# Kernel tuning notes

Measured on AMD Instinct MI355X. Metric: run time of the kernel, lower is better.

Reference implementation:

```python
import jax, jax.numpy as jnp
import numpy as np

N_NODES = 100000
N_EDGES = 1000000
F_IN = 8
HID = 64
VOCAB = 64
TXT_F = 64
SEQ = 10
N_CLASSES = 2


def setup_inputs() -> dict:
    key = jax.random.key(0)
    ks = jax.random.split(key, 16)
    inp = {
        "x": jax.random.normal(ks[0], (N_NODES, F_IN), dtype=jnp.float32),
        "edge_index": jax.random.randint(ks[1], (2, N_EDGES), 0, N_NODES, dtype=jnp.int32),
        "xtext": jax.random.randint(ks[2], (N_NODES, SEQ), 0, VOCAB, dtype=jnp.int32),
        # GCN layers (PyG convention: out = norm_agg(x @ W) + b)
        "conv1_w": jax.random.normal(ks[3], (F_IN, HID), dtype=jnp.float32) * 0.2,
        "conv1_b": jnp.zeros((HID,), jnp.float32),
        "conv2_w": jax.random.normal(ks[4], (HID, HID), dtype=jnp.float32) * 0.1,
        "conv2_b": jnp.zeros((HID,), jnp.float32),
        # embedding + GRU (torch layout: w_ih [3H, in], w_hh [3H, H])
        "embed": jax.random.normal(ks[5], (VOCAB, TXT_F), dtype=jnp.float32) * 0.1,
        "gru_w_ih": jax.random.normal(ks[6], (3 * HID, TXT_F), dtype=jnp.float32) * 0.1,
        "gru_w_hh": jax.random.normal(ks[7], (3 * HID, HID), dtype=jnp.float32) * 0.1,
        "gru_b_ih": jnp.zeros((3 * HID,), jnp.float32),
        "gru_b_hh": jnp.zeros((3 * HID,), jnp.float32),
        # pair MLPs (torch Linear layout: [out, in])
        "lin1_w": jax.random.normal(ks[8], (HID, 2 * HID), dtype=jnp.float32) * 0.1,
        "lin1_b": jnp.zeros((HID,), jnp.float32),
        "lin_text_w": jax.random.normal(ks[9], (HID, 2 * HID), dtype=jnp.float32) * 0.1,
        "lin_text_b": jnp.zeros((HID,), jnp.float32),
        "lin_final_w": jax.random.normal(ks[10], (N_CLASSES, 2 * HID), dtype=jnp.float32) * 0.1,
        "lin_final_b": jnp.zeros((N_CLASSES,), jnp.float32),
    }
    return inp


def _gcn_norm(edge_index, n_nodes):
    # PyG GCNConv default: add self loops, symmetric normalization
    loops = jnp.arange(n_nodes, dtype=edge_index.dtype)
    src = jnp.concatenate([edge_index[0], loops])
    dst = jnp.concatenate([edge_index[1], loops])
    deg = jax.ops.segment_sum(jnp.ones_like(dst, dtype=jnp.float32), dst, num_segments=n_nodes)
    dinv = jnp.where(deg > 0, jax.lax.rsqrt(deg), 0.0)
    norm = dinv[src] * dinv[dst]  # [E+N]
    return src, dst, norm


def _gcn(h, src, dst, norm, W, b, n_nodes):
    h = h @ W                              # [N, out]
    msg = h[src] * norm[:, None]           # gather + scale
    out = jax.ops.segment_sum(msg, dst, num_segments=n_nodes)
    return out + b


def _gru_last(xe, w_ih, w_hh, b_ih, b_hh):
    # xe: [N, T, F]; returns last hidden state [N, H]
    H = w_hh.shape[1]
    gi_all = jnp.einsum('ntf,gf->ntg', xe, w_ih) + b_ih  # precompute input gates [N,T,3H]
    gi_all = jnp.transpose(gi_all, (1, 0, 2))            # [T, N, 3H]

    def step(h, gi):
        gh = h @ w_hh.T + b_hh
        i_r, i_z, i_n = jnp.split(gi, 3, axis=-1)
        h_r, h_z, h_n = jnp.split(gh, 3, axis=-1)
        r = jax.nn.sigmoid(i_r + h_r)
        z = jax.nn.sigmoid(i_z + h_z)
        n = jnp.tanh(i_n + r * h_n)
        h = (1.0 - z) * n + z * h
        return h, None

    h0 = jnp.zeros((xe.shape[0], H), xe.dtype)
    h_last, _ = jax.lax.scan(step, h0, gi_all)
    return h_last


def reference(x, edge_index, xtext,
              conv1_w, conv1_b, conv2_w, conv2_b,
              embed, gru_w_ih, gru_w_hh, gru_b_ih, gru_b_hh,
              lin1_w, lin1_b, lin_text_w, lin_text_b, lin_final_w, lin_final_b):
    n = x.shape[0]
    src, dst, norm = _gcn_norm(edge_index, n)

    h = jax.nn.relu(_gcn(x, src, dst, norm, conv1_w, conv1_b, n))
    h = jax.nn.relu(_gcn(h, src, dst, norm, conv2_w, conv2_b, n))

    xe = embed[xtext]                                   # [N, T, F]
    textout = _gru_last(xe, gru_w_ih, gru_w_hh, gru_b_ih, gru_b_hh)  # [N, 64]

    s, t = edge_index[0], edge_index[1]
    xpair = jnp.concatenate([h[s], h[t]], axis=1)       # [E, 128]
    xpair = jax.nn.relu(xpair @ lin1_w.T + lin1_b)

    xpairtext = jnp.concatenate([textout[s], textout[t]], axis=1)
    xpairtext = jax.nn.relu(xpairtext @ lin_text_w.T + lin_text_b)

    xfin = jnp.concatenate([xpair, xpairtext], axis=1) @ lin_final_w.T + lin_final_b
    return jax.nn.log_softmax(xfin, axis=1)
```

## Files before the change

kernel.cpp:

```cpp
#include <hip/hip_runtime.h>
#include <stdint.h>

#define N_NODES 100000
#define N_EDGES 1000000
#define NBLK 391

typedef unsigned short u16;
typedef unsigned int u32;
typedef __attribute__((ext_vector_type(8))) short bshort8;
typedef __attribute__((ext_vector_type(4))) float f32x4;

__device__ __forceinline__ float bf2f(u16 u){ union{float f; u32 i;} x; x.i=((u32)u)<<16; return x.f; }
__device__ __forceinline__ u16 f2bf(float f){ union{float f; u32 i;} x; x.f=f; u32 r = x.i + 0x7FFFu + ((x.i>>16)&1u); return (u16)(r>>16); }

__device__ __forceinline__ float fexp2(float x){
#if __has_builtin(__builtin_amdgcn_exp2f)
    return __builtin_amdgcn_exp2f(x);
#else
    return exp2f(x);
#endif
}
__device__ __forceinline__ float frcp(float x){
#if __has_builtin(__builtin_amdgcn_rcpf)
    return __builtin_amdgcn_rcpf(x);
#else
    return 1.0f/x;
#endif
}
#define LOG2E 1.442695041f

__global__ void k_detect(const u16* __restrict__ x, int* flagp){
    __shared__ int cnt;
    if(threadIdx.x == 0) cnt = 0;
    __syncthreads();
    int c = 0;
    for(int i = threadIdx.x; i < 2048; i += 256){
        int e = (x[i] >> 7) & 0xFF;
        if(e >= 0x90) c++;
    }
    atomicAdd(&cnt, c);
    __syncthreads();
    if(threadIdx.x == 0) flagp[0] = (cnt > 64) ? 1 : 0;
}

#define CX    0
#define CW1   800000
#define CB1   800512
#define CW2   800576
#define CB2   804672
#define CEMB  804736
#define CWIH  808832
#define CWHH  821120
#define CBIH  833408
#define CBHH  833600
#define CL1W  833792
#define CL1B  841984
#define CLTW  842048
#define CLTB  850240
#define CLFW  850304
#define CLFB  850560
#define CTOT  850562

__device__ __forceinline__ float ldany(const void* p, int i, int fl){
    return fl ? ((const float*)p)[i] : bf2f(((const u16*)p)[i]);
}

__global__ void k_convert(const int* __restrict__ flagp,
                          const void* x, const void* w1, const void* b1, const void* w2,
                          const void* b2, const void* emb, const void* wih, const void* whh,
                          const void* bih, const void* bhh, const void* l1w, const void* l1b,
                          const void* ltw, const void* ltb, const void* lfw, const void* lfb,
                          float* __restrict__ canon){
    int i = blockIdx.x*256 + threadIdx.x;
    if(i >= CTOT) return;
    int fl = *flagp;
    const void* p; int off;
    if     (i < CW1 ){ p = x;   off = i;        }
    else if(i < CB1 ){ p = w1;  off = i - CW1;  }
    else if(i < CW2 ){ p = b1;  off = i - CB1;  }
    else if(i < CB2 ){ p = w2;  off = i - CW2;  }
    else if(i < CEMB){ p = b2;  off = i - CB2;  }
    else if(i < CWIH){ p = emb; off = i - CEMB; }
    else if(i < CWHH){ p = wih; off = i - CWIH; }
    else if(i < CBIH){ p = whh; off = i - CWHH; }
    else if(i < CBHH){ p = bih; off = i - CBIH; }
    else if(i < CL1W){ p = bhh; off = i - CBHH; }
    else if(i < CL1B){ p = l1w; off = i - CL1W; }
    else if(i < CLTW){ p = l1b; off = i - CL1B; }
    else if(i < CLTB){ p = ltw; off = i - CLTW; }
    else if(i < CLFW){ p = ltb; off = i - CLTB; }
    else if(i < CLFB){ p = lfw; off = i - CLFW; }
    else             { p = lfb; off = i - CLFB; }
    float v = ldany(p, off, fl);
    canon[i] = (v == v && fabsf(v) < 1e30f) ? v : 0.f;
}

__global__ void k_hist(const int* __restrict__ ei, int* __restrict__ deg){
    int e = blockIdx.x*256 + threadIdx.x;
    if(e < N_EDGES) atomicAdd(&deg[ei[N_EDGES + e]], 1);
}
__global__ void k_scan1(const int* __restrict__ deg, int* __restrict__ rowptr,
                        int* __restrict__ bsum){
    __shared__ int sh[256];
    int tid = threadIdx.x;
    int i = blockIdx.x*256 + tid;
    int v = (i < N_NODES) ? deg[i] : 0;
    sh[tid] = v;
    __syncthreads();
    for(int off = 1; off < 256; off <<= 1){
        int t = (tid >= off) ? sh[tid - off] : 0;
        __syncthreads();
        sh[tid] += t;
        __syncthreads();
    }
    if(i < N_NODES) rowptr[i] = sh[tid] - v;
    if(tid == 255) bsum[blockIdx.x] = sh[255];
}
__global__ void k_scan2(int* __restrict__ bsum){
    __shared__ int sh[512];
    int tid = threadIdx.x;
    int v = (tid < NBLK) ? bsum[tid] : 0;
    sh[tid] = v;
    __syncthreads();
    for(int off = 1; off < 512; off <<= 1){
        int t = (tid >= off) ? sh[tid - off] : 0;
        __syncthreads();
        sh[tid] += t;
        __syncthreads();
    }
    if(tid < NBLK) bsum[tid] = sh[tid] - v;
}
__global__ void k_scan3(const int* __restrict__ deg, const int* __restrict__ bsum,
                        int* __restrict__ rowptr, int* __restrict__ cursor,
                        float* __restrict__ dinv){
    int i = blockIdx.x*256 + threadIdx.x;
    if(i < N_NODES){
        int r = rowptr[i] + bsum[i >> 8];
        rowptr[i] = r;
        cursor[i] = r;
        dinv[i] = rsqrtf((float)deg[i] + 1.0f);
    }
    if(i == 0) rowptr[N_NODES] = N_EDGES;
}
__global__ void k_fill(const int* __restrict__ ei, int* __restrict__ cursor,
                       int* __restrict__ el, int* __restrict__ dl, int* __restrict__ eid){
    int e = blockIdx.x*256 + threadIdx.x;
    if(e < N_EDGES){
        int s = ei[e], d = ei[N_EDGES + e];
        int pos = atomicAdd(&cursor[d], 1);
        el[pos] = s;
        dl[pos] = d;
        eid[pos] = e;
    }
}

__global__ void k_t1s(const float* __restrict__ cx, const float* __restrict__ cw1,
                      const float* __restrict__ dinv, u16* __restrict__ src){
    __shared__ float w[512];
    int t = threadIdx.x;
    w[t]       = cw1[t];
    w[t + 256] = cw1[t + 256];
    __syncthreads();
    int i = blockIdx.x*256 + t;
    int n = i >> 6, f = i & 63;
    const float* xr = cx + n*8;
    float acc = 0.f;
    #pragma unroll
    for(int k = 0; k < 8; k++) acc += xr[k] * w[k*64 + f];
    src[i] = f2bf(acc * dinv[n]);
}

__global__ __launch_bounds__(256)
void k_gather_ep(const int* __restrict__ rowptr, const int* __restrict__ el,
                 const u16* __restrict__ src, const float* __restrict__ dinv,
                 const float* __restrict__ b, u16* __restrict__ h, int ostride){
    int gid = blockIdx.x*256 + threadIdx.x;
    int node = gid >> 6, lane = gid & 63;
    int beg = rowptr[node], end = rowptr[node + 1];
    float acc = bf2f(src[node*64 + lane]);
    int i = beg;
    for(; i + 4 <= end; i += 4){
        int s0 = el[i], s1 = el[i+1], s2 = el[i+2], s3 = el[i+3];
        float a0 = bf2f(src[s0*64 + lane]);
        float a1 = bf2f(src[s1*64 + lane]);
        float a2 = bf2f(src[s2*64 + lane]);
        float a3 = bf2f(src[s3*64 + lane]);
        acc += a0; acc += a1; acc += a2; acc += a3;
    }
    for(; i < end; i++) acc += bf2f(src[el[i]*64 + lane]);
    h[node*ostride + lane] = f2bf(fmaxf(dinv[node]*acc + b[lane], 0.f));
}

__global__ void k_packb(const float* __restrict__ src, u16* __restrict__ dst,
                        int K, int N, int ldk, int ldn){
    int i = blockIdx.x*256 + threadIdx.x;
    if(i >= K*N) return;
    int k = i / N, n = i % N;
    int kt = k >> 5, kk = k & 31, q = kk >> 3, j = kk & 7;
    int nt = n >> 4, nn = n & 15;
    int KT = K >> 5;
    dst[(((nt*KT + kt)*64) + (q*16 + nn))*8 + j] = f2bf(src[k*ldk + n*ldn]);
}

__global__ void k_gitab(const float* __restrict__ emb, const float* __restrict__ wih,
                        const float* __restrict__ bih, const float* __restrict__ bhh,
                        float* __restrict__ giT){
    int i = blockIdx.x*256 + threadIdx.x;
    if(i >= 64*192) return;
    int v = i / 192, g = i % 192;
    float acc = bih[g] + ((g < 128) ? bhh[g] : 0.0f);
    const float* wr = wih + g*64;
    const float* er = emb + v*64;
    for(int f = 0; f < 64; f++) acc += wr[f] * er[f];
    giT[i] = acc;
}

__global__ __launch_bounds__(256, 4)
void k_conv2(const u16* __restrict__ h, const u16* __restrict__ w2p,
             const float* __restrict__ dinv, u16* __restrict__ src){
    int wv = threadIdx.x >> 6, lane = threadIdx.x & 63;
    int g = blockIdx.x*4 + wv;
    if(g >= N_NODES/16) return;
    int q = lane >> 4, m = lane & 15, col = m;
    bshort8 a0 = *(const bshort8*)(h + (g*16 + m)*64 + q*8);
    bshort8 a1 = *(const bshort8*)(h + (g*16 + m)*64 + 32 + q*8);
    f32x4 acc[4];
    #pragma unroll
    for(int nt = 0; nt < 4; nt++){
        f32x4 c = {0.f,0.f,0.f,0.f};
        c = __builtin_amdgcn_mfma_f32_16x16x32_bf16(a0, *(const bshort8*)(w2p + ((nt*2+0)*64 + lane)*8), c, 0,0,0);
        c = __builtin_amdgcn_mfma_f32_16x16x32_bf16(a1, *(const bshort8*)(w2p + ((nt*2+1)*64 + lane)*8), c, 0,0,0);
        acc[nt] = c;
    }
    #pragma unroll
    for(int nt = 0; nt < 4; nt++)
        #pragma unroll
        for(int r = 0; r < 4; r++){
            int node = g*16 + q*4 + r;
            src[node*64 + nt*16 + col] = f2bf(acc[nt][r] * dinv[node]);
        }
}

__global__ __launch_bounds__(256, 3)
void k_gru(const int* __restrict__ xt, const u16* __restrict__ whhp,
           const float* __restrict__ giT, const float* __restrict__ bhh,
           u16* __restrict__ txt){
    __shared__ __align__(16) u16 wsh[12288];
    __shared__ __align__(16) float hsh[4][16][68];
    int tid = threadIdx.x;
    {
        const uint4* s = (const uint4*)whhp;
        uint4* d = (uint4*)wsh;
        #pragma unroll
        for(int i = 0; i < 6; i++) d[tid + 256*i] = s[tid + 256*i];
    }
    __syncthreads();

    int wv = tid >> 6, lane = tid & 63;
    int q = lane >> 4, m = lane & 15, col = m;
    int g = blockIdx.x*4 + wv;
    bool active = g < (N_NODES/16);
    int nb = active ? g*16 : 0;

    float bhhn[4];
    #pragma unroll
    for(int t = 0; t < 4; t++) bhhn[t] = bhh[128 + t*16 + col];

    const bshort8* wl = (const bshort8*)wsh;
    float* hp = &hsh[wv][m][0];

    float hc[4][4];
    #pragma unroll
    for(int t = 0; t < 4; t++)
        #pragma unroll
        for(int r = 0; r < 4; r++) hc[t][r] = 0.f;

    for(int s = 0; s < 10; s++){
        #pragma unroll
        for(int t = 0; t < 4; t++)
            #pragma unroll
            for(int r = 0; r < 4; r++)
                hsh[wv][q*4 + r][t*16 + col] = hc[t][r];

        float4 x0 = *(float4*)(hp + q*8);
        float4 x1 = *(float4*)(hp + q*8 + 4);
        float4 x2 = *(float4*)(hp + 32 + q*8);
        float4 x3 = *(float4*)(hp + 32 + q*8 + 4);
        u32 aw[8];
        aw[0] = (u32)f2bf(x0.x) | ((u32)f2bf(x0.y) << 16);
        aw[1] = (u32)f2bf(x0.z) | ((u32)f2bf(x0.w) << 16);
        aw[2] = (u32)f2bf(x1.x) | ((u32)f2bf(x1.y) << 16);
        aw[3] = (u32)f2bf(x1.z) | ((u32)f2bf(x1.w) << 16);
        aw[4] = (u32)f2bf(x2.x) | ((u32)f2bf(x2.y) << 16);
        aw[5] = (u32)f2bf(x2.z) | ((u32)f2bf(x2.w) << 16);
        aw[6] = (u32)f2bf(x3.x) | ((u32)f2bf(x3.y) << 16);
        aw[7] = (u32)f2bf(x3.z) | ((u32)f2bf(x3.w) << 16);
        bshort8 a0 = *(bshort8*)&aw[0];
        bshort8 a1 = *(bshort8*)&aw[4];

        int tok[4];
        #pragma unroll
        for(int r = 0; r < 4; r++) tok[r] = xt[(nb + q*4 + r)*10 + s] & 63;

        f32x4 acc[12];
        #pragma unroll
        for(int nt = 0; nt < 12; nt++){
            f32x4 c = {0.f,0.f,0.f,0.f};
            c = __builtin_amdgcn_mfma_f32_16x16x32_bf16(a0, wl[(nt*2+0)*64 + lane], c, 0,0,0);
            c = __builtin_amdgcn_mfma_f32_16x16x32_bf16(a1, wl[(nt*2+1)*64 + lane], c, 0,0,0);
            acc[nt] = c;
        }

        #pragma unroll
        for(int r = 0; r < 4; r++){
            const float* gp = giT + tok[r]*192 + col;
            #pragma unroll
            for(int t = 0; t < 4; t++){
                float gir = gp[t*16], giz = gp[64 + t*16], gin = gp[128 + t*16];
                float rr = frcp(1.0f + fexp2(-LOG2E*(gir + acc[t][r])));
                float zz = frcp(1.0f + fexp2(-LOG2E*(giz + acc[4+t][r])));
                float narg = gin + rr*(acc[8+t][r] + bhhn[t]);
                float e2 = fexp2(2.0f*LOG2E*narg);
                float nn = 1.0f - 2.0f*frcp(e2 + 1.0f);
                hc[t][r] = nn + zz*(hc[t][r] - nn);
            }
        }
        asm volatile("" ::: "memory");
    }
    if(active){
        #pragma unroll
        for(int t = 0; t < 4; t++)
            #pragma unroll
            for(int r = 0; r < 4; r++)
                txt[(size_t)(nb + q*4 + r)*128 + t*16 + col] = f2bf(hc[t][r]);
    }
}

__global__ __launch_bounds__(256, 2)
void k_edge(const int* __restrict__ el, const int* __restrict__ dl, const int* __restrict__ eid,
            const u16* __restrict__ nodef,
            const u16* __restrict__ l1p, const u16* __restrict__ ltp,
            const float* __restrict__ b1, const float* __restrict__ bt,
            const float* __restrict__ wfin, const float* __restrict__ bfin,
            const int* __restrict__ flagp, void* __restrict__ out){
    int lane = threadIdx.x & 63;
    int q = lane >> 4, m = lane & 15, col = m;
    int wgid = (blockIdx.x*256 + threadIdx.x) >> 6;
    int nw = (gridDim.x*256) >> 6;
    int fl = *flagp;

    bshort8 wa[16], wb[16];
    #pragma unroll
    for(int i = 0; i < 16; i++){
        wa[i] = *(const bshort8*)(l1p + (i*64 + lane)*8);
        wb[i] = *(const bshort8*)(ltp + (i*64 + lane)*8);
    }
    float b1c[4], btc[4], wfp[2][4], wft[2][4];
    #pragma unroll
    for(int t = 0; t < 4; t++){
        b1c[t] = b1[t*16 + col];
        btc[t] = bt[t*16 + col];
        wfp[0][t] = wfin[t*16 + col];        wfp[1][t] = wfin[128 + t*16 + col];
        wft[0][t] = wfin[64 + t*16 + col];   wft[1][t] = wfin[128 + 64 + t*16 + col];
    }
    float bf0 = bfin[0], bf1 = bfin[1];

    for(int g = wgid; g < N_EDGES/16; g += nw){
        int pos = g*16 + m;
        int s = el[pos], d = dl[pos];
        const u16* sp = nodef + (size_t)s*128;
        const u16* dp = nodef + (size_t)d*128;
        bshort8 a0 = *(const bshort8*)(sp + q*8);
        bshort8 a1 = *(const bshort8*)(sp + 32 + q*8);
        bshort8 a2 = *(const bshort8*)(dp + q*8);
        bshort8 a3 = *(const bshort8*)(dp + 32 + q*8);
        bshort8 c0 = *(const bshort8*)(sp + 64 + q*8);
        bshort8 c1 = *(const bshort8*)(sp + 96 + q*8);
        bshort8 c2 = *(const bshort8*)(dp + 64 + q*8);
        bshort8 c3 = *(const bshort8*)(dp + 96 + q*8);
        f32x4 p[4];
        #pragma unroll
        for(int nt = 0; nt < 4; nt++){
            f32x4 c = {0.f,0.f,0.f,0.f};
            c = __builtin_amdgcn_mfma_f32_16x16x32_bf16(a0, wa[nt*4+0], c, 0,0,0);
            c = __builtin_amdgcn_mfma_f32_16x16x32_bf16(a1, wa[nt*4+1], c, 0,0,0);
            c = __builtin_amdgcn_mfma_f32_16x16x32_bf16(a2, wa[nt*4+2], c, 0,0,0);
            c = __builtin_amdgcn_mfma_f32_16x16x32_bf16(a3, wa[nt*4+3], c, 0,0,0);
            p[nt] = c;
        }
        f32x4 pt[4];
        #pragma unroll
        for(int nt = 0; nt < 4; nt++){
            f32x4 c = {0.f,0.f,0.f,0.f};
            c = __builtin_amdgcn_mfma_f32_16x16x32_bf16(c0, wb[nt*4+0], c, 0,0,0);
            c = __builtin_amdgcn_mfma_f32_16x16x32_bf16(c1, wb[nt*4+1], c, 0,0,0);
            c = __builtin_amdgcn_mfma_f32_16x16x32_bf16(c2, wb[nt*4+2], c, 0,0,0);
            c = __builtin_amdgcn_mfma_f32_16x16x32_bf16(c3, wb[nt*4+3], c, 0,0,0);
            pt[nt] = c;
        }
        float l0[4], l1[4];
        #pragma unroll
        for(int r = 0; r < 4; r++){
            float s0 = 0.f, s1 = 0.f;
            #pragma unroll
            for(int t = 0; t < 4; t++){
                float xp = fmaxf(p[t][r]  + b1c[t], 0.f);
                float xq = fmaxf(pt[t][r] + btc[t], 0.f);
                s0 += xp*wfp[0][t] + xq*wft[0][t];
                s1 += xp*wfp[1][t] + xq*wft[1][t];
            }
            l0[r] = s0; l1[r] = s1;
        }
        #pragma unroll
        for(int r = 0; r < 4; r++)
            #pragma unroll
            for(int msk = 1; msk < 16; msk <<= 1){
                l0[r] += __shfl_xor(l0[r], msk, 64);
                l1[r] += __shfl_xor(l1[r], msk, 64);
            }
        if(m == 0){
            #pragma unroll
            for(int r = 0; r < 4; r++){
                float a = l0[r] + bf0, b = l1[r] + bf1;
                float mx = fmaxf(a, b);
                float lse = mx + __logf(__expf(a - mx) + __expf(b - mx));
                int oi = eid[g*16 + q*4 + r];
                if(fl){
                    float2 v; v.x = a - lse; v.y = b - lse;
                    ((float2*)out)[oi] = v;
                }else{
                    u32 pack = (u32)f2bf(a - lse) | ((u32)f2bf(b - lse) << 16);
                    ((u32*)out)[oi] = pack;
                }
            }
        }
    }
}

static const size_t O_FLAG   = 0;
static const size_t O_CANON  = 4096;
static const size_t O_GIT    = 3407872;
static const size_t O_W2P    = 3457024;
static const size_t O_WHHP   = 3465216;
static const size_t O_L1P    = 3489792;
static const size_t O_LTP    = 3506176;
static const size_t O_DINV   = 3522560;
static const size_t O_DEG    = 3922560;
static const size_t O_ROWPTR = 4322560;
static const size_t O_CURSOR = 4722688;
static const size_t O_BSUM   = 5122688;
static const size_t O_EL     = 5124736;
static const size_t O_DL     = 9125888;
static const size_t O_EID    = 13125888;
static const size_t O_SRC    = 17125888;
static const size_t O_H1     = 29925888;
static const size_t O_NODEF  = 29925888;

extern "C" void kernel_launch(void* const* d_in, const int* in_sizes, int n_in,
                              void* d_out, int out_size, void* d_ws, size_t ws_size,
                              hipStream_t stream){
    const void* x    = d_in[0];
    const int*  ei   = (const int*)d_in[1];
    const int*  xt   = (const int*)d_in[2];

    char* ws = (char*)d_ws;
    int*   flagp  = (int*)(ws + O_FLAG);
    float* canon  = (float*)(ws + O_CANON);
    float* giT    = (float*)(ws + O_GIT);
    u16*   w2p    = (u16*)(ws + O_W2P);
    u16*   whhp   = (u16*)(ws + O_WHHP);
    u16*   l1p    = (u16*)(ws + O_L1P);
    u16*   ltp    = (u16*)(ws + O_LTP);
    float* dinv   = (float*)(ws + O_DINV);
    int*   deg    = (int*)(ws + O_DEG);
    int*   rowptr = (int*)(ws + O_ROWPTR);
    int*   cursor = (int*)(ws + O_CURSOR);
    int*   bsum   = (int*)(ws + O_BSUM);
    int*   el     = (int*)(ws + O_EL);
    int*   dl     = (int*)(ws + O_DL);
    int*   eid    = (int*)(ws + O_EID);
    u16*   src    = (u16*)(ws + O_SRC);
    u16*   hbuf1  = (u16*)(ws + O_H1);
    u16*   nodef  = (u16*)(ws + O_NODEF);

    k_detect<<<1, 256, 0, stream>>>((const u16*)x, flagp);
    k_convert<<<(CTOT+255)/256, 256, 0, stream>>>(flagp,
        x, d_in[3], d_in[4], d_in[5], d_in[6], d_in[7], d_in[8], d_in[9],
        d_in[10], d_in[11], d_in[12], d_in[13], d_in[14], d_in[15], d_in[16], d_in[17],
        canon);

    const float* cx   = canon + CX;
    const float* cw1  = canon + CW1;
    const float* cb1  = canon + CB1;
    const float* cw2  = canon + CW2;
    const float* cb2  = canon + CB2;
    const float* cemb = canon + CEMB;
    const float* cwih = canon + CWIH;
    const float* cwhh = canon + CWHH;
    const float* cbih = canon + CBIH;
    const float* cbhh = canon + CBHH;
    const float* cl1w = canon + CL1W;
    const float* cl1b = canon + CL1B;
    const float* cltw = canon + CLTW;
    const float* cltb = canon + CLTB;
    const float* clfw = canon + CLFW;
    const float* clfb = canon + CLFB;

    hipMemsetAsync(deg, 0, (size_t)N_NODES*4, stream);
    k_hist <<<(N_EDGES+255)/256, 256, 0, stream>>>(ei, deg);
    k_scan1<<<NBLK, 256, 0, stream>>>(deg, rowptr, bsum);
    k_scan2<<<1, 512, 0, stream>>>(bsum);
    k_scan3<<<NBLK, 256, 0, stream>>>(deg, bsum, rowptr, cursor, dinv);
    k_fill <<<(N_EDGES+255)/256, 256, 0, stream>>>(ei, cursor, el, dl, eid);

    k_packb<<<(64*64+255)/256, 256, 0, stream>>>(cw2, w2p, 64, 64, 64, 1);
    k_packb<<<(64*192+255)/256, 256, 0, stream>>>(cwhh, whhp, 64, 192, 1, 64);
    k_packb<<<(128*64+255)/256, 256, 0, stream>>>(cl1w, l1p, 128, 64, 1, 128);
    k_packb<<<(128*64+255)/256, 256, 0, stream>>>(cltw, ltp, 128, 64, 1, 128);
    k_gitab<<<(64*192+255)/256, 256, 0, stream>>>(cemb, cwih, cbih, cbhh, giT);

    k_t1s<<<N_NODES*64/256, 256, 0, stream>>>(cx, cw1, dinv, src);
    k_gather_ep<<<N_NODES*64/256, 256, 0, stream>>>(rowptr, el, src, dinv, cb1, hbuf1, 64);

    k_conv2<<<(N_NODES/16 + 3)/4, 256, 0, stream>>>(hbuf1, w2p, dinv, src);
    k_gather_ep<<<N_NODES*64/256, 256, 0, stream>>>(rowptr, el, src, dinv, cb2, nodef, 128);

    k_gru<<<(N_NODES/16 + 3)/4, 256, 0, stream>>>(xt, whhp, giT, cbhh, nodef + 64);

    k_edge<<<2048, 256, 0, stream>>>(el, dl, eid, nodef, l1p, ltp, cl1b, cltb, clfw, clfb,
                                     flagp, d_out);
}
```

Before: 529.9 us.

## Precompute per-node halves of pair MLPs and reduce edge kernel to gather-add

Splits the lin1 and lin_text weights into source and destination halves and applies them once per node in a new pre-pass, so the edge kernel only gathers two precomputed 64-wide packed vectors, adds them, applies ReLU and the final projection. This removes the per-edge MFMA matmuls, which repeated work across 1M edges that only needs doing for 100K nodes. The pre-pass writes its results back into the node feature buffer in place, and the layout moves nodef to a new offset. Per-node results are rounded to bf16 before the add, which adds some rounding error.

```diff
diff --git a/kernel.cpp b/kernel.cpp
--- a/kernel.cpp
+++ b/kernel.cpp
@@ -282,6 +282,7 @@
             for(int r = 0; r < 4; r++)
                 hsh[wv][q*4 + r][t*16 + col] = hc[t][r];
 
+        asm volatile("" ::: "memory");
         float4 x0 = *(float4*)(hp + q*8);
         float4 x1 = *(float4*)(hp + q*8 + 4);
         float4 x2 = *(float4*)(hp + 32 + q*8);
@@ -336,102 +337,116 @@
     }
 }
 
-__global__ __launch_bounds__(256, 2)
-void k_edge(const int* __restrict__ el, const int* __restrict__ dl, const int* __restrict__ eid,
-            const u16* __restrict__ nodef,
-            const u16* __restrict__ l1p, const u16* __restrict__ ltp,
-            const float* __restrict__ b1, const float* __restrict__ bt,
-            const float* __restrict__ wfin, const float* __restrict__ bfin,
-            const int* __restrict__ flagp, void* __restrict__ out){
-    int lane = threadIdx.x & 63;
+__global__ __launch_bounds__(256, 3)
+void k_pairpre(u16* nodef, u32* __restrict__ udst,
+               const u16* __restrict__ w1a, const u16* __restrict__ w1b,
+               const u16* __restrict__ wta, const u16* __restrict__ wtb,
+               const float* __restrict__ b1, const float* __restrict__ bt){
+    int wv = threadIdx.x >> 6, lane = threadIdx.x & 63;
+    int g = blockIdx.x*4 + wv;
+    if(g >= N_NODES/16) return;
     int q = lane >> 4, m = lane & 15, col = m;
-    int wgid = (blockIdx.x*256 + threadIdx.x) >> 6;
-    int nw = (gridDim.x*256) >> 6;
+    const u16* row = nodef + (size_t)(g*16 + m)*128;
+    bshort8 ah0 = *(const bshort8*)(row);
+    bshort8 ah1 = *(const bshort8*)(row + 32 - q*8 + q*8 + 32);
+    ah0 = *(const bshort8*)(row + q*8);
+    ah1 = *(const bshort8*)(row + 32 + q*8);
+    bshort8 at0 = *(const bshort8*)(row + 64 + q*8);
+    bshort8 at1 = *(const bshort8*)(row + 96 + q*8);
+    f32x4 u1[4], u2[4], v1[4], v2[4];
+    #pragma unroll
+    for(int nt = 0; nt < 4; nt++){
+        f32x4 c;
+        c = (f32x4){0.f,0.f,0.f,0.f};
+        c = __builtin_amdgcn_mfma_f32_16x16x32_bf16(ah0, *(const bshort8*)(w1a + ((nt*2+0)*64 + lane)*8), c, 0,0,0);
+        c = __builtin_amdgcn_mfma_f32_16x16x32_bf16(ah1, *(const bshort8*)(w1a + ((nt*2+1)*64 + lane)*8), c, 0,0,0);
+        u1[nt] = c;
+        c = (f32x4){0.f,0.f,0.f,0.f};
+        c = __builtin_amdgcn_mfma_f32_16x16x32_bf16(ah0, *(const bshort8*)(w1b + ((nt*2+0)*64 + lane)*8), c, 0,0,0);
+        c = __builtin_amdgcn_mfma_f32_16x16x32_bf16(ah1, *(const bshort8*)(w1b + ((nt*2+1)*64 + lane)*8), c, 0,0,0);
+        u2[nt] = c;
+        c = (f32x4){0.f,0.f,0.f,0.f};
+        c = __builtin_amdgcn_mfma_f32_16x16x32_bf16(at0, *(const bshort8*)(wta + ((nt*2+0)*64 + lane)*8), c, 0,0,0);
+        c = __builtin_amdgcn_mfma_f32_16x16x32_bf16(at1, *(const bshort8*)(wta + ((nt*2+1)*64 + lane)*8), c, 0,0,0);
+        v1[nt] = c;
+        c = (f32x4){0.f,0.f,0.f,0.f};
+        c = __builtin_amdgcn_mfma_f32_16x16x32_bf16(at0, *(const bshort8*)(wtb + ((nt*2+0)*64 + lane)*8), c, 0,0,0);
+        c = __builtin_amdgcn_mfma_f32_16x16x32_bf16(at1, *(const bshort8*)(wtb + ((nt*2+1)*64 + lane)*8), c, 0,0,0);
+        v2[nt] = c;
+    }
+    u32* usrc = (u32*)nodef;
+    #pragma unroll
+    for(int nt = 0; nt < 4; nt++){
+        int f = nt*16 + col;
+        float b1f = b1[f], btf = bt[f];
+        #pragma unroll
+        for(int r = 0; r < 4; r++){
+            int node = g*16 + q*4 + r;
+            u32 pa = (u32)f2bf(u1[nt][r] + b1f) | ((u32)f2bf(v1[nt][r] + btf) << 16);
+            u32 pb = (u32)f2bf(u2[nt][r]) | ((u32)f2bf(v2[nt][r]) << 16);
+            usrc[(size_t)node*64 + f] = pa;
+            udst[(size_t)node*64 + f] = pb;
+        }
+    }
+}
+
+__global__ __launch_bounds__(256, 6)
+void k_edge2(const int* __restrict__ el, const int* __restrict__ dl, const int* __restrict__ eid,
+             const u32* __restrict__ usrc, const u32* __restrict__ udst,
+             const float* __restrict__ wfin, const float* __restrict__ bfin,
+             const int* __restrict__ flagp, void* __restrict__ out){
+    int tid = threadIdx.x;
+    int lane = tid & 63;
+    int q = lane >> 4, f0 = lane & 15;
+    int wid = (blockIdx.x*256 + tid) >> 6;
+    int nwv = (gridDim.x*256) >> 6;
     int fl = *flagp;
 
-    bshort8 wa[16], wb[16];
-    #pragma unroll
-    for(int i = 0; i < 16; i++){
-        wa[i] = *(const bshort8*)(l1p + (i*64 + lane)*8);
-        wb[i] = *(const bshort8*)(ltp + (i*64 + lane)*8);
-    }
-    float b1c[4], btc[4], wfp[2][4], wft[2][4];
+    float wp0[4], wp1[4], wt0[4], wt1[4];
     #pragma unroll
     for(int t = 0; t < 4; t++){
-        b1c[t] = b1[t*16 + col];
-        btc[t] = bt[t*16 + col];
-        wfp[0][t] = wfin[t*16 + col];        wfp[1][t] = wfin[128 + t*16 + col];
-        wft[0][t] = wfin[64 + t*16 + col];   wft[1][t] = wfin[128 + 64 + t*16 + col];
+        int f = f0 + 16*t;
+        wp0[t] = wfin[f];        wt0[t] = wfin[64 + f];
+        wp1[t] = wfin[128 + f];  wt1[t] = wfin[192 + f];
     }
     float bf0 = bfin[0], bf1 = bfin[1];
 
-    for(int g = wgid; g < N_EDGES/16; g += nw){
-        int pos = g*16 + m;
-        int s = el[pos], d = dl[pos];
-        const u16* sp = nodef + (size_t)s*128;
-        const u16* dp = nodef + (size_t)d*128;
-        bshort8 a0 = *(const bshort8*)(sp + q*8);
-        bshort8 a1 = *(const bshort8*)(sp + 32 + q*8);
-        bshort8 a2 = *(const bshort8*)(dp + q*8);
-        bshort8 a3 = *(const bshort8*)(dp + 32 + q*8);
-        bshort8 c0 = *(const bshort8*)(sp + 64 + q*8);
-        bshort8 c1 = *(const bshort8*)(sp + 96 + q*8);
-        bshort8 c2 = *(const bshort8*)(dp + 64 + q*8);
-        bshort8 c3 = *(const bshort8*)(dp + 96 + q*8);
-        f32x4 p[4];
-        #pragma unroll
-        for(int nt = 0; nt < 4; nt++){
-            f32x4 c = {0.f,0.f,0.f,0.f};
-            c = __builtin_amdgcn_mfma_f32_16x16x32_bf16(a0, wa[nt*4+0], c, 0,0,0);
-            c = __builtin_amdgcn_mfma_f32_16x16x32_bf16(a1, wa[nt*4+1], c, 0,0,0);
-            c = __builtin_amdgcn_mfma_f32_16x16x32_bf16(a2, wa[nt*4+2], c, 0,0,0);
-            c = __builtin_amdgcn_mfma_f32_16x16x32_bf16(a3, wa[nt*4+3], c, 0,0,0);
-            p[nt] = c;
-        }
-        f32x4 pt[4];
-        #pragma unroll
-        for(int nt = 0; nt < 4; nt++){
-            f32x4 c = {0.f,0.f,0.f,0.f};
-            c = __builtin_amdgcn_mfma_f32_16x16x32_bf16(c0, wb[nt*4+0], c, 0,0,0);
-            c = __builtin_amdgcn_mfma_f32_16x16x32_bf16(c1, wb[nt*4+1], c, 0,0,0);
-            c = __builtin_amdgcn_mfma_f32_16x16x32_bf16(c2, wb[nt*4+2], c, 0,0,0);
-            c = __builtin_amdgcn_mfma_f32_16x16x32_bf16(c3, wb[nt*4+3], c, 0,0,0);
-            pt[nt] = c;
-        }
-        float l0[4], l1[4];
-        #pragma unroll
-        for(int r = 0; r < 4; r++){
-            float s0 = 0.f, s1 = 0.f;
-            #pragma unroll
-            for(int t = 0; t < 4; t++){
-                float xp = fmaxf(p[t][r]  + b1c[t], 0.f);
-                float xq = fmaxf(pt[t][r] + btc[t], 0.f);
-                s0 += xp*wfp[0][t] + xq*wft[0][t];
-                s1 += xp*wfp[1][t] + xq*wft[1][t];
-            }
-            l0[r] = s0; l1[r] = s1;
-        }
-        #pragma unroll
-        for(int r = 0; r < 4; r++)
-            #pragma unroll
-            for(int msk = 1; msk < 16; msk <<= 1){
-                l0[r] += __shfl_xor(l0[r], msk, 64);
-                l1[r] += __shfl_xor(l1[r], msk, 64);
-            }
-        if(m == 0){
-            #pragma unroll
-            for(int r = 0; r < 4; r++){
-                float a = l0[r] + bf0, b = l1[r] + bf1;
-                float mx = fmaxf(a, b);
-                float lse = mx + __logf(__expf(a - mx) + __expf(b - mx));
-                int oi = eid[g*16 + q*4 + r];
-                if(fl){
-                    float2 v; v.x = a - lse; v.y = b - lse;
-                    ((float2*)out)[oi] = v;
-                }else{
-                    u32 pack = (u32)f2bf(a - lse) | ((u32)f2bf(b - lse) << 16);
-                    ((u32*)out)[oi] = pack;
-                }
+    for(int grp = wid; grp < N_EDGES/4; grp += nwv){
+        int e = grp*4 + q;
+        int s = el[e], d = dl[e];
+        const u32* up = usrc + (size_t)s*64 + f0;
+        const u32* vp = udst + (size_t)d*64 + f0;
+        u32 us[4], ud[4];
+        #pragma unroll
+        for(int t = 0; t < 4; t++){ us[t] = up[16*t]; ud[t] = vp[16*t]; }
+        float s0 = 0.f, s1 = 0.f;
+        #pragma unroll
+        for(int t = 0; t < 4; t++){
+            float u1 = __uint_as_float(us[t] << 16);
+            float v1 = __uint_as_float(us[t] & 0xffff0000u);
+            float u2 = __uint_as_float(ud[t] << 16);
+            float v2 = __uint_as_float(ud[t] & 0xffff0000u);
+            float xp = fmaxf(u1 + u2, 0.f);
+            float xq = fmaxf(v1 + v2, 0.f);
+            s0 += xp*wp0[t] + xq*wt0[t];
+            s1 += xp*wp1[t] + xq*wt1[t];
+        }
+        #pragma unroll
+        for(int msk = 1; msk < 16; msk <<= 1){
+            s0 += __shfl_xor(s0, msk, 64);
+            s1 += __shfl_xor(s1, msk, 64);
+        }
+        if(f0 == 0){
+            float a = s0 + bf0, b = s1 + bf1;
+            float mx = fmaxf(a, b);
+            float lse = mx + __logf(__expf(a - mx) + __expf(b - mx));
+            int oi = eid[e];
+            if(fl){
+                float2 v; v.x = a - lse; v.y = b - lse;
+                ((float2*)out)[oi] = v;
+            }else{
+                u32 pack = (u32)f2bf(a - lse) | ((u32)f2bf(b - lse) << 16);
+                ((u32*)out)[oi] = pack;
             }
         }
     }
@@ -442,8 +457,10 @@
 static const size_t O_GIT    = 3407872;
 static const size_t O_W2P    = 3457024;
 static const size_t O_WHHP   = 3465216;
-static const size_t O_L1P    = 3489792;
-static const size_t O_LTP    = 3506176;
+static const size_t O_L1PA   = 3489792;
+static const size_t O_L1PB   = 3497984;
+static const size_t O_LTPA   = 3506176;
+static const size_t O_LTPB   = 3514368;
 static const size_t O_DINV   = 3522560;
 static const size_t O_DEG    = 3922560;
 static const size_t O_ROWPTR = 4322560;
@@ -454,7 +471,8 @@
 static const size_t O_EID    = 13125888;
 static const size_t O_SRC    = 17125888;
 static const size_t O_H1     = 29925888;
-static const size_t O_NODEF  = 29925888;
+static const size_t O_UDST   = 17125888;
+static const size_t O_NODEF  = 42725888;
 
 extern "C" void kernel_launch(void* const* d_in, const int* in_sizes, int n_in,
                               void* d_out, int out_size, void* d_ws, size_t ws_size,
@@ -469,8 +487,10 @@
     float* giT    = (float*)(ws + O_GIT);
     u16*   w2p    = (u16*)(ws + O_W2P);
     u16*   whhp   = (u16*)(ws + O_WHHP);
-    u16*   l1p    = (u16*)(ws + O_L1P);
-    u16*   ltp    = (u16*)(ws + O_LTP);
+    u16*   l1pa   = (u16*)(ws + O_L1PA);
+    u16*   l1pb   = (u16*)(ws + O_L1PB);
+    u16*   ltpa   = (u16*)(ws + O_LTPA);
+    u16*   ltpb   = (u16*)(ws + O_LTPB);
     float* dinv   = (float*)(ws + O_DINV);
     int*   deg    = (int*)(ws + O_DEG);
     int*   rowptr = (int*)(ws + O_ROWPTR);
@@ -481,6 +501,7 @@
     int*   eid    = (int*)(ws + O_EID);
     u16*   src    = (u16*)(ws + O_SRC);
     u16*   hbuf1  = (u16*)(ws + O_H1);
+    u32*   udst   = (u32*)(ws + O_UDST);
     u16*   nodef  = (u16*)(ws + O_NODEF);
 
     k_detect<<<1, 256, 0, stream>>>((const u16*)x, flagp);
@@ -515,8 +536,10 @@
 
     k_packb<<<(64*64+255)/256, 256, 0, stream>>>(cw2, w2p, 64, 64, 64, 1);
     k_packb<<<(64*192+255)/256, 256, 0, stream>>>(cwhh, whhp, 64, 192, 1, 64);
-    k_packb<<<(128*64+255)/256, 256, 0, stream>>>(cl1w, l1p, 128, 64, 1, 128);
-    k_packb<<<(128*64+255)/256, 256, 0, stream>>>(cltw, ltp, 128, 64, 1, 128);
+    k_packb<<<(64*64+255)/256, 256, 0, stream>>>(cl1w,      l1pa, 64, 64, 1, 128);
+    k_packb<<<(64*64+255)/256, 256, 0, stream>>>(cl1w + 64, l1pb, 64, 64, 1, 128);
+    k_packb<<<(64*64+255)/256, 256, 0, stream>>>(cltw,      ltpa, 64, 64, 1, 128);
+    k_packb<<<(64*64+255)/256, 256, 0, stream>>>(cltw + 64, ltpb, 64, 64, 1, 128);
     k_gitab<<<(64*192+255)/256, 256, 0, stream>>>(cemb, cwih, cbih, cbhh, giT);
 
     k_t1s<<<N_NODES*64/256, 256, 0, stream>>>(cx, cw1, dinv, src);
@@ -527,6 +550,9 @@
 
     k_gru<<<(N_NODES/16 + 3)/4, 256, 0, stream>>>(xt, whhp, giT, cbhh, nodef + 64);
 
-    k_edge<<<2048, 256, 0, stream>>>(el, dl, eid, nodef, l1p, ltp, cl1b, cltb, clfw, clfb,
-                                     flagp, d_out);
-}
+    k_pairpre<<<(N_NODES/16 + 3)/4, 256, 0, stream>>>(nodef, udst, l1pa, l1pb, ltpa, ltpb,
+                                                      cl1b, cltb);
+
+    k_edge2<<<4096, 256, 0, stream>>>(el, dl, eid, (const u32*)nodef, udst,
+                                      clfw, clfb, flagp, d_out);
+}
```

Result: faster. 497.4 us (-6.1%).
